# Kernel optimization log

Measured on AMD Instinct MI355X. Metric: run time of the kernel, lower is better.

The kernel has to match this reference:

```python
import jax, jax.numpy as jnp
import numpy as np

B, M, W, C, NN, J, ED, EMB = 8, 4096, 128, 32, 16, 4, 5, 2
EPS = 1e-5


def setup_inputs() -> dict:
    key = jax.random.key(0)
    ks = jax.random.split(key, 30)
    s = 0.05
    x = jax.random.normal(ks[0], (B, M, W), jnp.float32)
    pseudo = jax.random.normal(ks[1], (M * NN, EMB), jnp.float32)
    # structured indices: row r scatters its NN attention weights into row r of the m x m matrix
    nbr = jax.random.randint(ks[2], (M, NN), 0, M)
    L_idx = (jnp.arange(M)[:, None] * M + nbr).reshape(-1).astype(jnp.int32)
    inp = dict(x=x, pseudo=pseudo, L_idx=L_idx)
    inp['edge_w'] = jax.random.normal(ks[3], (ED, EMB), jnp.float32) * s
    inp['edge_b'] = jnp.zeros((ED,), jnp.float32)
    # Gaussian mixture params per layer (J components, encode_dim each); reset_parameters -> N(0,1)
    inp['mu0'] = jax.random.normal(ks[4], (J, ED), jnp.float32)
    inp['sigma0'] = jax.random.normal(ks[5], (J, ED), jnp.float32)
    inp['mu1'] = jax.random.normal(ks[6], (J, ED), jnp.float32)
    inp['sigma1'] = jax.random.normal(ks[7], (J, ED), jnp.float32)
    # layer 0: W -> C ; layer 1: C -> C
    inp['l1w0'] = jax.random.normal(ks[8], (C, W), jnp.float32) * s
    inp['l1b0'] = jnp.zeros((C,), jnp.float32)
    inp['l2w0'] = jax.random.normal(ks[9], (C, W), jnp.float32) * s
    inp['l2b0'] = jnp.zeros((C,), jnp.float32)
    inp['l1w1'] = jax.random.normal(ks[10], (C, C), jnp.float32) * s
    inp['l1b1'] = jnp.zeros((C,), jnp.float32)
    inp['l2w1'] = jax.random.normal(ks[11], (C, C), jnp.float32) * s
    inp['l2b1'] = jnp.zeros((C,), jnp.float32)
    inp['bn_g0'] = jnp.ones((C,), jnp.float32)
    inp['bn_b0'] = jnp.zeros((C,), jnp.float32)
    inp['bn_g1'] = jnp.ones((C,), jnp.float32)
    inp['bn_b1'] = jnp.zeros((C,), jnp.float32)
    inp['fc1w'] = jax.random.normal(ks[12], (256, M * C), jnp.float32) * 0.005
    inp['fc1b'] = jnp.zeros((256,), jnp.float32)
    inp['fc2w'] = jax.random.normal(ks[13], (53, 256), jnp.float32) * s
    inp['fc2b'] = jnp.zeros((53,), jnp.float32)
    return inp


def _get_L(pseudo, L_idx, edge_w, edge_b, mu, sigma, dtype):
    # Gaussian-mixture edge attention: u^T diag(sigma) u per component, summed, exp(-0.5 *)
    emb = pseudo @ edge_w.T + edge_b                      # (E, ED), E = M*NN
    u = emb[None, :, :] - mu[:, None, :]                  # (J, E, ED)
    q = jnp.sum(u * u * sigma[:, None, :], axis=-1)       # (J, E)
    w = jnp.sum(jnp.exp(-0.5 * q), axis=0)                # (E,)
    attn = jax.nn.softmax(w.reshape(M, NN), axis=1).reshape(-1)
    return jnp.zeros(M * M, dtype).at[L_idx].set(attn).reshape(M, M)


def _layer(x, L, w1, b1, w2, b2, g, bb):
    Lx = jnp.einsum('mn,bnf->bmf', L, x)                  # graph conv
    h = Lx @ w1.T + b1 + x @ w2.T + b2                    # (B, M, C)
    # BatchNorm1d (training mode): stats over batch and node dims, biased variance
    mean = jnp.mean(h, axis=(0, 1))
    var = jnp.var(h, axis=(0, 1))
    h = (h - mean) * jax.lax.rsqrt(var + EPS) * g + bb
    return jax.nn.relu(h)


def reference(x, pseudo, L_idx, edge_w, edge_b, mu0, sigma0, mu1, sigma1,
              l1w0, l1b0, l2w0, l2b0, l1w1, l1b1, l2w1, l2b1,
              bn_g0, bn_b0, bn_g1, bn_b1, fc1w, fc1b, fc2w, fc2b):
    L0 = _get_L(pseudo, L_idx, edge_w, edge_b, mu0, sigma0, x.dtype)
    h = _layer(x, L0, l1w0, l1b0, l2w0, l2b0, bn_g0, bn_b0)
    L1 = _get_L(pseudo, L_idx, edge_w, edge_b, mu1, sigma1, x.dtype)
    h = _layer(h, L1, l1w1, l1b1, l2w1, l2b1, bn_g1, bn_b1)
    flat = h.reshape(B, M * C)
    out = jax.nn.relu(flat @ fc1w.T + fc1b)               # dropout = identity (eval)
    return out @ fc2w.T + fc2b                            # (B, 53)
```

## Files before the change

### kernel.cpp

```cpp
#include <hip/hip_runtime.h>
#include <hip/hip_cooperative_groups.h>

namespace cg = cooperative_groups;

#define B_ 8
#define M_ 4096
#define W_ 128
#define C_ 32
#define NN_ 16

typedef short s16x8 __attribute__((ext_vector_type(8)));
typedef float f32x4 __attribute__((ext_vector_type(4)));

static __device__ __forceinline__ unsigned short f2bf(float f) {
  unsigned u = __builtin_bit_cast(unsigned, f);
  u = u + 0x7FFFu + ((u >> 16) & 1u);
  return (unsigned short)(u >> 16);
}
static __device__ __forceinline__ s16x8 cvt8v(float4 a, float4 b) {
  s16x8 r;
  r[0] = (short)f2bf(a.x); r[1] = (short)f2bf(a.y);
  r[2] = (short)f2bf(a.z); r[3] = (short)f2bf(a.w);
  r[4] = (short)f2bf(b.x); r[5] = (short)f2bf(b.y);
  r[6] = (short)f2bf(b.z); r[7] = (short)f2bf(b.w);
  return r;
}
static __device__ __forceinline__ float safeexp(float a) {
  return expf(fminf(a, 87.f));
}

__global__ void poison_kernel(float* __restrict__ out, int n, float val) {
  int t = blockIdx.x * blockDim.x + threadIdx.x;
  if (t < n) out[t] = val;
}


static __device__ void attn_row(
    int m, const float* __restrict__ pseudo, const int* __restrict__ Lidx,
    const float* __restrict__ edge_w, const float* __restrict__ edge_b,
    const float* __restrict__ mu0, const float* __restrict__ sg0,
    const float* __restrict__ mu1, const float* __restrict__ sg1,
    float* __restrict__ we0, float* __restrict__ we1, int* __restrict__ colb) {
  float w0[NN_], w1[NN_];
  int col[NN_];
#pragma unroll
  for (int n = 0; n < NN_; n++) {
    int e = m * NN_ + n;
    float p0 = pseudo[e * 2], p1 = pseudo[e * 2 + 1];
    float emb[5];
#pragma unroll
    for (int d = 0; d < 5; d++)
      emb[d] = p0 * edge_w[d * 2] + p1 * edge_w[d * 2 + 1] + edge_b[d];
    float a0 = 0.f, a1 = 0.f;
#pragma unroll
    for (int j = 0; j < 4; j++) {
      float qa = 0.f, qb = 0.f;
#pragma unroll
      for (int d = 0; d < 5; d++) {
        float u0 = emb[d] - mu0[j * 5 + d];
        qa += u0 * u0 * sg0[j * 5 + d];
        float u1 = emb[d] - mu1[j * 5 + d];
        qb += u1 * u1 * sg1[j * 5 + d];
      }
      a0 += safeexp(-0.5f * qa);
      a1 += safeexp(-0.5f * qb);
    }
    w0[n] = a0; w1[n] = a1;
    col[n] = Lidx[e] % M_;
  }
  float mx0 = w0[0], mx1 = w1[0];
#pragma unroll
  for (int n = 1; n < NN_; n++) { mx0 = fmaxf(mx0, w0[n]); mx1 = fmaxf(mx1, w1[n]); }
  float s0 = 0.f, s1 = 0.f;
#pragma unroll
  for (int n = 0; n < NN_; n++) {
    w0[n] = safeexp(w0[n] - mx0); s0 += w0[n];
    w1[n] = safeexp(w1[n] - mx1); s1 += w1[n];
  }
  float r0 = 1.f / s0, r1 = 1.f / s1;
#pragma unroll
  for (int n = 0; n < NN_; n++) {
    bool last = true;
#pragma unroll
    for (int n2 = n + 1; n2 < NN_; n2++)
      if (col[n2] == col[n]) last = false;
    int e = m * NN_ + n;
    we0[e] = last ? w0[n] * r0 : 0.f;
    we1[e] = last ? w1[n] * r1 : 0.f;
    colb[e] = col[n];
  }
}

static __device__ void proj0_tile(
    int blk, int tid, const float* __restrict__ x, const float* __restrict__ l1w0,
    const float* __restrict__ l2w0, float* __restrict__ G) {
  int lane = tid & 63, wave = tid >> 6;
  int l16 = lane & 15, quad = lane >> 4;
  int tile = blk * 4 + wave;
  f32x4 acc[4];
#pragma unroll
  for (int ct = 0; ct < 4; ct++) acc[ct] = (f32x4){0.f, 0.f, 0.f, 0.f};
  int row = tile * 16 + l16;
  const float* xr = x + (size_t)row * 128 + quad * 8;
  int out0 = l16;
#pragma unroll
  for (int kit = 0; kit < 4; kit++) {
    const float* ap = xr + kit * 32;
    s16x8 a = cvt8v(*(const float4*)ap, *(const float4*)(ap + 4));
#pragma unroll
    for (int ct = 0; ct < 4; ct++) {
      int out = ct * 16 + out0;
      const float* src = (out < 32 ? l1w0 + out * 128 : l2w0 + (out - 32) * 128)
                         + kit * 32 + quad * 8;
      s16x8 bf = cvt8v(*(const float4*)src, *(const float4*)(src + 4));
      acc[ct] = __builtin_amdgcn_mfma_f32_16x16x32_bf16(a, bf, acc[ct], 0, 0, 0);
    }
  }
  int rbase = tile * 16 + quad * 4;
#pragma unroll
  for (int ct = 0; ct < 4; ct++)
#pragma unroll
    for (int i = 0; i < 4; i++)
      G[(size_t)(rbase + i) * 64 + ct * 16 + l16] = acc[ct][i];
}

static __device__ void conv_block(
    int cb, int tid, char* smem,
    const float* __restrict__ G, const float* __restrict__ we,
    const int* __restrict__ colb, const float* __restrict__ b1c,
    const float* __restrict__ b2c, float* __restrict__ h,
    float* __restrict__ bns, float* __restrict__ bnq) {
  float (*s_we)[16] = (float(*)[16])smem;
  int   (*s_cn)[16] = (int(*)[16])(smem + 512);
  float* s_s = (float*)(smem + 1024);
  float* s_q = (float*)(smem + 1152);
  if (tid < 128) {
    int row = tid >> 4, nn = tid & 15;
    int m = (cb * 8 + row) & 4095;
    s_we[row][nn] = we[m * 16 + nn];
    s_cn[row][nn] = colb[m * 16 + nn];
  } else if (tid < 160) {
    s_s[tid - 128] = 0.f;
    s_q[tid - 128] = 0.f;
  }
  __syncthreads();
  int row = tid >> 5, c = tid & 31;
  int r = cb * 8 + row;
  int b = r >> 12;
  const float* Gb = G + ((size_t)b << 18);
  float acc = 0.f;
#pragma unroll
  for (int nn = 0; nn < NN_; nn++)
    acc += s_we[row][nn] * Gb[s_cn[row][nn] * 64 + c];
  float hv = acc + G[(size_t)r * 64 + 32 + c] + b1c[c] + b2c[c];
  h[(size_t)r * 32 + c] = hv;
  atomicAdd(&s_s[c], hv);
  atomicAdd(&s_q[c], hv * hv);
  __syncthreads();
  if (tid < 32) {
    int slot = cb & 255;
    atomicAdd(&bns[tid * 256 + slot], s_s[tid]);
    atomicAdd(&bnq[tid * 256 + slot], s_q[tid]);
  }
}

static __device__ void bnfin_block(
    int tid, char* smem, const float* __restrict__ bns, const float* __restrict__ bnq,
    const float* __restrict__ g, const float* __restrict__ bb,
    float* __restrict__ scale, float* __restrict__ shift) {
  float (*red)[8][32] = (float(*)[8][32])smem;
  int c = tid & 31, part = tid >> 5;
  float s = 0.f, q = 0.f;
#pragma unroll 8
  for (int i = 0; i < 32; i++) {
    s += bns[c * 256 + part * 32 + i];
    q += bnq[c * 256 + part * 32 + i];
  }
  red[0][part][c] = s;
  red[1][part][c] = q;
  __syncthreads();
  if (tid < 32) {
    float S = 0.f, Q = 0.f;
#pragma unroll
    for (int p = 0; p < 8; p++) { S += red[0][p][tid]; Q += red[1][p][tid]; }
    float mean = S * (1.f / 32768.f);
    float var = fmaxf(Q * (1.f / 32768.f) - mean * mean, 0.f);
    float sc = g[tid] * rsqrtf(var + 1e-5f);
    scale[tid] = sc;
    shift[tid] = bb[tid] - mean * sc;
  }
}

static __device__ void proj1_tile(
    int blk, int tid, const float* __restrict__ h0, const float* __restrict__ sc0,
    const float* __restrict__ l1w1, const float* __restrict__ l2w1,
    float* __restrict__ G) {
  int lane = tid & 63, wave = tid >> 6;
  int l16 = lane & 15, quad = lane >> 4;
  int tile = blk * 4 + wave;
  int row = tile * 16 + l16;
  const float* hr = h0 + (size_t)row * 32 + quad * 8;
  float4 hv0 = *(const float4*)hr;
  float4 hv1 = *(const float4*)(hr + 4);
  float av[8] = {hv0.x, hv0.y, hv0.z, hv0.w, hv1.x, hv1.y, hv1.z, hv1.w};
  s16x8 a;
#pragma unroll
  for (int j = 0; j < 8; j++) {
    float scv = sc0[quad * 8 + j];
    float shv = sc0[32 + quad * 8 + j];
    a[j] = (short)f2bf(fmaxf(av[j] * scv + shv, 0.f));
  }
  f32x4 acc[4];
#pragma unroll
  for (int ct = 0; ct < 4; ct++) {
    int out = ct * 16 + l16;
    const float* src = (out < 32 ? l1w1 + out * 32 : l2w1 + (out - 32) * 32) + quad * 8;
    s16x8 bf = cvt8v(*(const float4*)src, *(const float4*)(src + 4));
    f32x4 z = {0.f, 0.f, 0.f, 0.f};
    acc[ct] = __builtin_amdgcn_mfma_f32_16x16x32_bf16(a, bf, z, 0, 0, 0);
  }
  int rbase = tile * 16 + quad * 4;
#pragma unroll
  for (int ct = 0; ct < 4; ct++)
#pragma unroll
    for (int i = 0; i < 4; i++)
      G[(size_t)(rbase + i) * 64 + ct * 16 + l16] = acc[ct][i];
}

static __device__ void fc1_block(
    int u, int tid, char* smem, const float* __restrict__ h1,
    const float* __restrict__ sc1, const float* __restrict__ fc1w,
    float* __restrict__ fc1acc) {
  short* als = (short*)smem;
  int kc = u >> 2;
  int og = u & 3;
  size_t kbase = (size_t)kc << 9;
  for (int s = tid; s < 2048; s += 256) {
    int rowb = s >> 7;
    int k4 = (s & 127) << 2;
    short4 v4 = {0, 0, 0, 0};
    if (rowb < 8) {
      float4 hv = *(const float4*)(h1 + ((size_t)rowb << 17) + kbase + k4);
      int c = k4 & 31;
      float4 scv = *(const float4*)(sc1 + c);
      float4 shv = *(const float4*)(sc1 + 32 + c);
      v4.x = (short)f2bf(fmaxf(hv.x * scv.x + shv.x, 0.f));
      v4.y = (short)f2bf(fmaxf(hv.y * scv.y + shv.y, 0.f));
      v4.z = (short)f2bf(fmaxf(hv.z * scv.z + shv.z, 0.f));
      v4.w = (short)f2bf(fmaxf(hv.w * scv.w + shv.w, 0.f));
    }
    int byte = ((rowb << 10) + (k4 << 1)) ^ ((rowb & 7) << 4);
    *(short4*)((char*)als + byte) = v4;
  }
  __syncthreads();
  int lane = tid & 63, wave = tid >> 6;
  int l16 = lane & 15, quad = lane >> 4;
  int o = og * 64 + wave * 16 + l16;
  const float* wr = fc1w + (size_t)o * 131072 + kbase + quad * 8;
  int abase = (l16 << 10) + (quad << 4);
  int axor = (l16 & 7) << 4;
  f32x4 acc = {0.f, 0.f, 0.f, 0.f};
#pragma unroll 4
  for (int kk = 0; kk < 16; kk++) {
    const float* wp = wr + kk * 32;
    s16x8 bfr = cvt8v(*(const float4*)wp, *(const float4*)(wp + 4));
    s16x8 afr = *(const s16x8*)((const char*)als + ((abase + (kk << 6)) ^ axor));
    acc = __builtin_amdgcn_mfma_f32_16x16x32_bf16(afr, bfr, acc, 0, 0, 0);
  }
  if (quad < 2) {
#pragma unroll
    for (int i = 0; i < 4; i++)
      atomicAdd(&fc1acc[(quad * 4 + i) * 256 + o], acc[i]);
  }
  __syncthreads();
}

static __device__ void fc2_elem(
    int t, const float* __restrict__ fc1acc, const float* __restrict__ fc2w,
    const float* __restrict__ fc2b, float* __restrict__ out) {
  int b = t / 53, j = t - b * 53;
  float s = fc2b[j];
  const float* fa = fc1acc + b * 256;
  const float* wr = fc2w + j * 256;
#pragma unroll 8
  for (int o = 0; o < 256; o++) s += fmaxf(fa[o], 0.f) * wr[o];
  out[t] = s;
}

static __device__ __forceinline__ void prefetch_q(
    const float* __restrict__ fc1w, int quarter, int idx, int stride) {
  const float4* p = (const float4*)fc1w + (size_t)quarter * 2097152;
  float acc = 0.f;
  for (int i = idx; i < 2097152; i += stride) {
    float4 v = p[i];
    acc += v.x + v.y + v.z + v.w;
  }
  asm volatile("" :: "v"(acc));
}

__global__ __launch_bounds__(256, 4) void fused_kernel(
    const float* __restrict__ x, const float* __restrict__ pseudo,
    const int* __restrict__ Lidx,
    const float* __restrict__ edge_w, const float* __restrict__ edge_b,
    const float* __restrict__ mu0, const float* __restrict__ sg0,
    const float* __restrict__ mu1, const float* __restrict__ sg1,
    const float* __restrict__ l1w0, const float* __restrict__ l1b0,
    const float* __restrict__ l2w0, const float* __restrict__ l2b0,
    const float* __restrict__ l1w1, const float* __restrict__ l1b1,
    const float* __restrict__ l2w1, const float* __restrict__ l2b1,
    const float* __restrict__ bng0, const float* __restrict__ bnb0,
    const float* __restrict__ bng1, const float* __restrict__ bnb1,
    const float* __restrict__ fc1w, const float* __restrict__ fc1b,
    const float* __restrict__ fc2w, const float* __restrict__ fc2b,
    float* __restrict__ out,
    int* __restrict__ colb, float* __restrict__ we0, float* __restrict__ we1,
    float* __restrict__ G, float* __restrict__ h,
    float* __restrict__ bn, float* __restrict__ sc, float* __restrict__ fc1acc) {
  __shared__ char smem[16384];
  cg::grid_group grid = cg::this_grid();
  int bid = blockIdx.x, tid = threadIdx.x;
  int gtid = bid * 256 + tid;

  if (gtid < 2048) fc1acc[gtid] = fc1b[gtid & 255];
  else if (gtid < 34816) bn[gtid - 2048] = 0.f;
  if (bid < 16)
    attn_row(gtid, pseudo, Lidx, edge_w, edge_b, mu0, sg0, mu1, sg1, we0, we1, colb);
  grid.sync();

  if (bid < 512) proj0_tile(bid, tid, x, l1w0, l2w0, G);
  else           prefetch_q(fc1w, 0, (bid - 512) * 256 + tid, 131072);
  grid.sync();

  for (int it = 0; it < 4; it++) {
    __syncthreads();
    conv_block(bid + it * 1024, tid, smem, G, we0, colb, l1b0, l2b0,
               h, bn, bn + 8192);
  }
  prefetch_q(fc1w, 1, gtid, 262144);
  grid.sync();

  if (bid == 0) bnfin_block(tid, smem, bn, bn + 8192, bng0, bnb0, sc, sc + 32);
  else          prefetch_q(fc1w, 2, gtid - 256, 261888);
  grid.sync();

  if (bid < 512) proj1_tile(bid, tid, h, sc, l1w1, l2w1, G);
  else           prefetch_q(fc1w, 3, (bid - 512) * 256 + tid, 131072);
  grid.sync();

  for (int it = 0; it < 4; it++) {
    __syncthreads();
    conv_block(bid + it * 1024, tid, smem, G, we1, colb, l1b1, l2b1,
               h, bn + 16384, bn + 24576);
  }
  grid.sync();

  if (bid == 0) bnfin_block(tid, smem, bn + 16384, bn + 24576, bng1, bnb1,
                            sc + 64, sc + 96);
  grid.sync();

  fc1_block(bid, tid, smem, h, sc + 64, fc1w, fc1acc);
  grid.sync();

  if (gtid < 424) fc2_elem(gtid, fc1acc, fc2w, fc2b, out);
}

__global__ __launch_bounds__(256) void init_kernel(
    float* __restrict__ fc1acc, const float* __restrict__ fc1b,
    float* __restrict__ bn) {
  int g = blockIdx.x * 256 + threadIdx.x;
  if (g < 2048) fc1acc[g] = fc1b[g & 255];
  else if (g < 34816) bn[g - 2048] = 0.f;
}

__global__ __launch_bounds__(256) void attn_kernel(
    const float* __restrict__ pseudo, const int* __restrict__ Lidx,
    const float* __restrict__ edge_w, const float* __restrict__ edge_b,
    const float* __restrict__ mu0, const float* __restrict__ sg0,
    const float* __restrict__ mu1, const float* __restrict__ sg1,
    float* __restrict__ we0, float* __restrict__ we1, int* __restrict__ colb) {
  int m = blockIdx.x * 256 + threadIdx.x;
  if (m < M_)
    attn_row(m, pseudo, Lidx, edge_w, edge_b, mu0, sg0, mu1, sg1, we0, we1, colb);
}

__global__ __launch_bounds__(256) void proj0_kernel(
    const float* __restrict__ x, const float* __restrict__ l1w0,
    const float* __restrict__ l2w0, float* __restrict__ G) {
  proj0_tile(blockIdx.x, threadIdx.x, x, l1w0, l2w0, G);
}

__global__ __launch_bounds__(256) void conv_kernel(
    const float* __restrict__ G,
    const float* __restrict__ we, const int* __restrict__ colb,
    const float* __restrict__ b1c, const float* __restrict__ b2c,
    float* __restrict__ h, float* __restrict__ bns, float* __restrict__ bnq) {
  __shared__ char smem[1280];
  conv_block(blockIdx.x, threadIdx.x, smem, G, we, colb, b1c, b2c, h, bns, bnq);
}

__global__ __launch_bounds__(256) void bnfin_kernel(
    const float* __restrict__ bns, const float* __restrict__ bnq,
    const float* __restrict__ g, const float* __restrict__ bb,
    float* __restrict__ scale, float* __restrict__ shift) {
  __shared__ char smem[2048];
  bnfin_block(threadIdx.x, smem, bns, bnq, g, bb, scale, shift);
}

__global__ __launch_bounds__(256) void proj1_kernel(
    const float* __restrict__ h0, const float* __restrict__ sc0,
    const float* __restrict__ l1w1, const float* __restrict__ l2w1,
    float* __restrict__ G) {
  proj1_tile(blockIdx.x, threadIdx.x, h0, sc0, l1w1, l2w1, G);
}

__global__ __launch_bounds__(256) void fc1_kernel(
    const float* __restrict__ h1, const float* __restrict__ sc1,
    const float* __restrict__ fc1w, float* __restrict__ fc1acc) {
  __shared__ char smem[16384];
  fc1_block(blockIdx.x, threadIdx.x, smem, h1, sc1, fc1w, fc1acc);
}

__global__ void fc2_kernel(const float* __restrict__ fc1acc,
                           const float* __restrict__ fc2w,
                           const float* __restrict__ fc2b,
                           float* __restrict__ out) {
  int t = blockIdx.x * blockDim.x + threadIdx.x;
  if (t < 424) fc2_elem(t, fc1acc, fc2w, fc2b, out);
}

extern "C" void kernel_launch(void* const* d_in, const int* in_sizes, int n_in,
                              void* d_out, int out_size, void* d_ws, size_t ws_size,
                              hipStream_t stream) {
  float* out = (float*)d_out;
  int bad = 0;
  if (n_in != 25) bad = 2;
  else if (in_sizes[0] != 4194304) bad = 3;
  else if (in_sizes[2] != 65536) bad = 4;
  else if (in_sizes[21] != 33554432) bad = 5;
  else if (out_size != 424) bad = 6;
  else if (ws_size < 13509120) bad = 1;
  if (bad) {
    poison_kernel<<<2, 256, 0, stream>>>(out, out_size, (float)bad * 1.0e6f);
    return;
  }

  const float* x      = (const float*)d_in[0];
  const float* pseudo = (const float*)d_in[1];
  const int*   Lidx   = (const int*)d_in[2];
  const float* edge_w = (const float*)d_in[3];
  const float* edge_b = (const float*)d_in[4];
  const float* mu0    = (const float*)d_in[5];
  const float* sg0    = (const float*)d_in[6];
  const float* mu1    = (const float*)d_in[7];
  const float* sg1    = (const float*)d_in[8];
  const float* l1w0   = (const float*)d_in[9];
  const float* l1b0   = (const float*)d_in[10];
  const float* l2w0   = (const float*)d_in[11];
  const float* l2b0   = (const float*)d_in[12];
  const float* l1w1   = (const float*)d_in[13];
  const float* l1b1   = (const float*)d_in[14];
  const float* l2w1   = (const float*)d_in[15];
  const float* l2b1   = (const float*)d_in[16];
  const float* bng0   = (const float*)d_in[17];
  const float* bnb0   = (const float*)d_in[18];
  const float* bng1   = (const float*)d_in[19];
  const float* bnb1   = (const float*)d_in[20];
  const float* fc1w   = (const float*)d_in[21];
  const float* fc1b   = (const float*)d_in[22];
  const float* fc2w   = (const float*)d_in[23];
  const float* fc2b   = (const float*)d_in[24];

  char* Wp = (char*)d_ws;
  int*   colb   = (int*)  (Wp + 0);
  float* we0    = (float*)(Wp + 262144);
  float* we1    = (float*)(Wp + 524288);
  float* G      = (float*)(Wp + 786432);
  float* h0     = (float*)(Wp + 9175040);
  float* bn     = (float*)(Wp + 13369344);
  float* sc     = (float*)(Wp + 13500416);
  float* fc1acc = (float*)(Wp + 13500928);

  int maxb = 0;
  hipError_t oe = hipOccupancyMaxActiveBlocksPerMultiprocessor(&maxb, fused_kernel, 256, 0);
  bool coop = (oe == hipSuccess && maxb >= 4);
  if (coop) {
    void* args[] = {
      (void*)&x, (void*)&pseudo, (void*)&Lidx, (void*)&edge_w, (void*)&edge_b,
      (void*)&mu0, (void*)&sg0, (void*)&mu1, (void*)&sg1,
      (void*)&l1w0, (void*)&l1b0, (void*)&l2w0, (void*)&l2b0,
      (void*)&l1w1, (void*)&l1b1, (void*)&l2w1, (void*)&l2b1,
      (void*)&bng0, (void*)&bnb0, (void*)&bng1, (void*)&bnb1,
      (void*)&fc1w, (void*)&fc1b, (void*)&fc2w, (void*)&fc2b,
      (void*)&out,
      (void*)&colb, (void*)&we0, (void*)&we1, (void*)&G, (void*)&h0,
      (void*)&bn, (void*)&sc, (void*)&fc1acc };
    hipError_t le = hipLaunchCooperativeKernel((const void*)fused_kernel,
                                               dim3(1024), dim3(256), args, 0, stream);
    if (le != hipSuccess) coop = false;
  }
  if (!coop) {
    init_kernel<<<136, 256, 0, stream>>>(fc1acc, fc1b, bn);
    attn_kernel<<<16, 256, 0, stream>>>(pseudo, Lidx, edge_w, edge_b,
                                        mu0, sg0, mu1, sg1, we0, we1, colb);
    proj0_kernel<<<512, 256, 0, stream>>>(x, l1w0, l2w0, G);
    conv_kernel<<<4096, 256, 0, stream>>>(G, we0, colb, l1b0, l2b0,
                                          h0, bn, bn + 8192);
    bnfin_kernel<<<1, 256, 0, stream>>>(bn, bn + 8192, bng0, bnb0, sc, sc + 32);
    proj1_kernel<<<512, 256, 0, stream>>>(h0, sc, l1w1, l2w1, G);
    conv_kernel<<<4096, 256, 0, stream>>>(G, we1, colb, l1b1, l2b1,
                                          h0, bn + 16384, bn + 24576);
    bnfin_kernel<<<1, 256, 0, stream>>>(bn + 16384, bn + 24576, bng1, bnb1,
                                        sc + 64, sc + 96);
    fc1_kernel<<<1024, 256, 0, stream>>>(h0, sc + 64, fc1w, fc1acc);
    fc2_kernel<<<2, 256, 0, stream>>>(fc1acc, fc2w, fc2b, out);
  }
}
```

Before: 340.6 us.

## Replace cooperative grid sync with custom atomic barrier and fewer grid phases

Drops the cooperative launch and cg grid.sync in favour of a hand-rolled generation-counter barrier, with counters zeroed by a separate init kernel. The number of grid-wide phases is cut: attention runs beside the first projection, and BatchNorm finalisation is recomputed redundantly in each block's shared memory instead of in a separate single-block phase. The fc1 weight prefetch is reorganised into two large sweeps. The barrier relies on all 1024 blocks being co-resident without a cooperative-launch guarantee, and its spin loop has a timeout that could break correctness if it expires.

```diff
diff --git a/kernel.cpp b/kernel.cpp
--- a/kernel.cpp
+++ b/kernel.cpp
@@ -1,13 +1,11 @@
 #include <hip/hip_runtime.h>
-#include <hip/hip_cooperative_groups.h>
-
-namespace cg = cooperative_groups;
 
 #define B_ 8
 #define M_ 4096
 #define W_ 128
 #define C_ 32
 #define NN_ 16
+#define NBLK 1024
 
 typedef short s16x8 __attribute__((ext_vector_type(8)));
 typedef float f32x4 __attribute__((ext_vector_type(4)));
@@ -32,6 +30,31 @@
 __global__ void poison_kernel(float* __restrict__ out, int n, float val) {
   int t = blockIdx.x * blockDim.x + threadIdx.x;
   if (t < n) out[t] = val;
+}
+
+static __device__ __forceinline__ void gridbar(unsigned* __restrict__ bar, int tid) {
+  __syncthreads();
+  if (tid == 0) {
+    unsigned* cnt = bar;
+    unsigned* gen = bar + 64;
+    unsigned g = __hip_atomic_load(gen, __ATOMIC_RELAXED, __HIP_MEMORY_SCOPE_AGENT);
+    __threadfence();
+    unsigned old = __hip_atomic_fetch_add(cnt, 1u, __ATOMIC_ACQ_REL,
+                                          __HIP_MEMORY_SCOPE_AGENT);
+    if (old == NBLK - 1) {
+      __hip_atomic_store(cnt, 0u, __ATOMIC_RELAXED, __HIP_MEMORY_SCOPE_AGENT);
+      __hip_atomic_fetch_add(gen, 1u, __ATOMIC_RELEASE, __HIP_MEMORY_SCOPE_AGENT);
+    } else {
+      int t = 0;
+      while (__hip_atomic_load(gen, __ATOMIC_ACQUIRE,
+                               __HIP_MEMORY_SCOPE_AGENT) == g) {
+        __builtin_amdgcn_s_sleep(4);
+        if (++t > (1 << 18)) break;
+      }
+    }
+    __threadfence();
+  }
+  __syncthreads();
 }
 
 
@@ -102,14 +125,13 @@
   for (int ct = 0; ct < 4; ct++) acc[ct] = (f32x4){0.f, 0.f, 0.f, 0.f};
   int row = tile * 16 + l16;
   const float* xr = x + (size_t)row * 128 + quad * 8;
-  int out0 = l16;
 #pragma unroll
   for (int kit = 0; kit < 4; kit++) {
     const float* ap = xr + kit * 32;
     s16x8 a = cvt8v(*(const float4*)ap, *(const float4*)(ap + 4));
 #pragma unroll
     for (int ct = 0; ct < 4; ct++) {
-      int out = ct * 16 + out0;
+      int out = ct * 16 + l16;
       const float* src = (out < 32 ? l1w0 + out * 128 : l2w0 + (out - 32) * 128)
                          + kit * 32 + quad * 8;
       s16x8 bf = cvt8v(*(const float4*)src, *(const float4*)(src + 4));
@@ -164,10 +186,10 @@
   }
 }
 
-static __device__ void bnfin_block(
+static __device__ void bnfin_local(
     int tid, char* smem, const float* __restrict__ bns, const float* __restrict__ bnq,
     const float* __restrict__ g, const float* __restrict__ bb,
-    float* __restrict__ scale, float* __restrict__ shift) {
+    float* __restrict__ s_sc) {
   float (*red)[8][32] = (float(*)[8][32])smem;
   int c = tid & 31, part = tid >> 5;
   float s = 0.f, q = 0.f;
@@ -186,9 +208,10 @@
     float mean = S * (1.f / 32768.f);
     float var = fmaxf(Q * (1.f / 32768.f) - mean * mean, 0.f);
     float sc = g[tid] * rsqrtf(var + 1e-5f);
-    scale[tid] = sc;
-    shift[tid] = bb[tid] - mean * sc;
-  }
+    s_sc[tid] = sc;
+    s_sc[32 + tid] = bb[tid] - mean * sc;
+  }
+  __syncthreads();
 }
 
 static __device__ void proj1_tile(
@@ -272,7 +295,6 @@
     for (int i = 0; i < 4; i++)
       atomicAdd(&fc1acc[(quad * 4 + i) * 256 + o], acc[i]);
   }
-  __syncthreads();
 }
 
 static __device__ void fc2_elem(
@@ -287,15 +309,23 @@
   out[t] = s;
 }
 
-static __device__ __forceinline__ void prefetch_q(
-    const float* __restrict__ fc1w, int quarter, int idx, int stride) {
-  const float4* p = (const float4*)fc1w + (size_t)quarter * 2097152;
+static __device__ __forceinline__ void prefetch_range(
+    const float4* __restrict__ p, int n, int idx, int stride) {
   float acc = 0.f;
-  for (int i = idx; i < 2097152; i += stride) {
+  for (int i = idx; i < n; i += stride) {
     float4 v = p[i];
     acc += v.x + v.y + v.z + v.w;
   }
   asm volatile("" :: "v"(acc));
+}
+
+__global__ __launch_bounds__(256) void init_kernel(
+    float* __restrict__ fc1acc, const float* __restrict__ fc1b,
+    float* __restrict__ bn, unsigned* __restrict__ bar) {
+  int g = blockIdx.x * 256 + threadIdx.x;
+  if (g < 2048) fc1acc[g] = fc1b[g & 255];
+  else if (g < 34816) bn[g - 2048] = 0.f;
+  else if (g < 34944) bar[g - 34816] = 0u;
 }
 
 __global__ __launch_bounds__(256, 4) void fused_kernel(
@@ -310,122 +340,56 @@
     const float* __restrict__ l2w1, const float* __restrict__ l2b1,
     const float* __restrict__ bng0, const float* __restrict__ bnb0,
     const float* __restrict__ bng1, const float* __restrict__ bnb1,
-    const float* __restrict__ fc1w, const float* __restrict__ fc1b,
-    const float* __restrict__ fc2w, const float* __restrict__ fc2b,
+    const float* __restrict__ fc1w, const float* __restrict__ fc2w,
+    const float* __restrict__ fc2b,
     float* __restrict__ out,
     int* __restrict__ colb, float* __restrict__ we0, float* __restrict__ we1,
     float* __restrict__ G, float* __restrict__ h,
-    float* __restrict__ bn, float* __restrict__ sc, float* __restrict__ fc1acc) {
-  __shared__ char smem[16384];
-  cg::grid_group grid = cg::this_grid();
+    float* __restrict__ bn, float* __restrict__ fc1acc,
+    unsigned* __restrict__ bar) {
+  __shared__ char smem[16640];
+  float* s_sc = (float*)(smem + 16384);
   int bid = blockIdx.x, tid = threadIdx.x;
-  int gtid = bid * 256 + tid;
-
-  if (gtid < 2048) fc1acc[gtid] = fc1b[gtid & 255];
-  else if (gtid < 34816) bn[gtid - 2048] = 0.f;
-  if (bid < 16)
-    attn_row(gtid, pseudo, Lidx, edge_w, edge_b, mu0, sg0, mu1, sg1, we0, we1, colb);
-  grid.sync();
-
-  if (bid < 512) proj0_tile(bid, tid, x, l1w0, l2w0, G);
-  else           prefetch_q(fc1w, 0, (bid - 512) * 256 + tid, 131072);
-  grid.sync();
+
+  if (bid < 512) {
+    proj0_tile(bid, tid, x, l1w0, l2w0, G);
+  } else if (bid < 528) {
+    attn_row((bid - 512) * 256 + tid, pseudo, Lidx, edge_w, edge_b,
+             mu0, sg0, mu1, sg1, we0, we1, colb);
+  } else {
+    prefetch_range((const float4*)fc1w, 4194304, (bid - 528) * 256 + tid, 126976);
+  }
+  gridbar(bar, tid);
 
   for (int it = 0; it < 4; it++) {
     __syncthreads();
     conv_block(bid + it * 1024, tid, smem, G, we0, colb, l1b0, l2b0,
                h, bn, bn + 8192);
   }
-  prefetch_q(fc1w, 1, gtid, 262144);
-  grid.sync();
-
-  if (bid == 0) bnfin_block(tid, smem, bn, bn + 8192, bng0, bnb0, sc, sc + 32);
-  else          prefetch_q(fc1w, 2, gtid - 256, 261888);
-  grid.sync();
-
-  if (bid < 512) proj1_tile(bid, tid, h, sc, l1w1, l2w1, G);
-  else           prefetch_q(fc1w, 3, (bid - 512) * 256 + tid, 131072);
-  grid.sync();
+  gridbar(bar, tid);
+
+  if (bid < 512) {
+    bnfin_local(tid, smem, bn, bn + 8192, bng0, bnb0, s_sc);
+    proj1_tile(bid, tid, h, s_sc, l1w1, l2w1, G);
+  } else {
+    prefetch_range((const float4*)fc1w + 4194304, 4194304,
+                   (bid - 512) * 256 + tid, 131072);
+  }
+  gridbar(bar, tid);
 
   for (int it = 0; it < 4; it++) {
     __syncthreads();
     conv_block(bid + it * 1024, tid, smem, G, we1, colb, l1b1, l2b1,
                h, bn + 16384, bn + 24576);
   }
-  grid.sync();
-
-  if (bid == 0) bnfin_block(tid, smem, bn + 16384, bn + 24576, bng1, bnb1,
-                            sc + 64, sc + 96);
-  grid.sync();
-
-  fc1_block(bid, tid, smem, h, sc + 64, fc1w, fc1acc);
-  grid.sync();
-
+  gridbar(bar, tid);
+
+  bnfin_local(tid, smem, bn + 16384, bn + 24576, bng1, bnb1, s_sc);
+  fc1_block(bid, tid, smem, h, s_sc, fc1w, fc1acc);
+  gridbar(bar, tid);
+
+  int gtid = bid * 256 + tid;
   if (gtid < 424) fc2_elem(gtid, fc1acc, fc2w, fc2b, out);
-}
-
-__global__ __launch_bounds__(256) void init_kernel(
-    float* __restrict__ fc1acc, const float* __restrict__ fc1b,
-    float* __restrict__ bn) {
-  int g = blockIdx.x * 256 + threadIdx.x;
-  if (g < 2048) fc1acc[g] = fc1b[g & 255];
-  else if (g < 34816) bn[g - 2048] = 0.f;
-}
-
-__global__ __launch_bounds__(256) void attn_kernel(
-    const float* __restrict__ pseudo, const int* __restrict__ Lidx,
-    const float* __restrict__ edge_w, const float* __restrict__ edge_b,
-    const float* __restrict__ mu0, const float* __restrict__ sg0,
-    const float* __restrict__ mu1, const float* __restrict__ sg1,
-    float* __restrict__ we0, float* __restrict__ we1, int* __restrict__ colb) {
-  int m = blockIdx.x * 256 + threadIdx.x;
-  if (m < M_)
-    attn_row(m, pseudo, Lidx, edge_w, edge_b, mu0, sg0, mu1, sg1, we0, we1, colb);
-}
-
-__global__ __launch_bounds__(256) void proj0_kernel(
-    const float* __restrict__ x, const float* __restrict__ l1w0,
-    const float* __restrict__ l2w0, float* __restrict__ G) {
-  proj0_tile(blockIdx.x, threadIdx.x, x, l1w0, l2w0, G);
-}
-
-__global__ __launch_bounds__(256) void conv_kernel(
-    const float* __restrict__ G,
-    const float* __restrict__ we, const int* __restrict__ colb,
-    const float* __restrict__ b1c, const float* __restrict__ b2c,
-    float* __restrict__ h, float* __restrict__ bns, float* __restrict__ bnq) {
-  __shared__ char smem[1280];
-  conv_block(blockIdx.x, threadIdx.x, smem, G, we, colb, b1c, b2c, h, bns, bnq);
-}
-
-__global__ __launch_bounds__(256) void bnfin_kernel(
-    const float* __restrict__ bns, const float* __restrict__ bnq,
-    const float* __restrict__ g, const float* __restrict__ bb,
-    float* __restrict__ scale, float* __restrict__ shift) {
-  __shared__ char smem[2048];
-  bnfin_block(threadIdx.x, smem, bns, bnq, g, bb, scale, shift);
-}
-
-__global__ __launch_bounds__(256) void proj1_kernel(
-    const float* __restrict__ h0, const float* __restrict__ sc0,
-    const float* __restrict__ l1w1, const float* __restrict__ l2w1,
-    float* __restrict__ G) {
-  proj1_tile(blockIdx.x, threadIdx.x, h0, sc0, l1w1, l2w1, G);
-}
-
-__global__ __launch_bounds__(256) void fc1_kernel(
-    const float* __restrict__ h1, const float* __restrict__ sc1,
-    const float* __restrict__ fc1w, float* __restrict__ fc1acc) {
-  __shared__ char smem[16384];
-  fc1_block(blockIdx.x, threadIdx.x, smem, h1, sc1, fc1w, fc1acc);
-}
-
-__global__ void fc2_kernel(const float* __restrict__ fc1acc,
-                           const float* __restrict__ fc2w,
-                           const float* __restrict__ fc2b,
-                           float* __restrict__ out) {
-  int t = blockIdx.x * blockDim.x + threadIdx.x;
-  if (t < 424) fc2_elem(t, fc1acc, fc2w, fc2b, out);
 }
 
 extern "C" void kernel_launch(void* const* d_in, const int* in_sizes, int n_in,
@@ -438,7 +402,7 @@
   else if (in_sizes[2] != 65536) bad = 4;
   else if (in_sizes[21] != 33554432) bad = 5;
   else if (out_size != 424) bad = 6;
-  else if (ws_size < 13509120) bad = 1;
+  else if (ws_size < 13509632) bad = 1;
   if (bad) {
     poison_kernel<<<2, 256, 0, stream>>>(out, out_size, (float)bad * 1.0e6f);
     return;
@@ -471,47 +435,19 @@
   const float* fc2b   = (const float*)d_in[24];
 
   char* Wp = (char*)d_ws;
-  int*   colb   = (int*)  (Wp + 0);
-  float* we0    = (float*)(Wp + 262144);
-  float* we1    = (float*)(Wp + 524288);
-  float* G      = (float*)(Wp + 786432);
-  float* h0     = (float*)(Wp + 9175040);
-  float* bn     = (float*)(Wp + 13369344);
-  float* sc     = (float*)(Wp + 13500416);
-  float* fc1acc = (float*)(Wp + 13500928);
-
-  int maxb = 0;
-  hipError_t oe = hipOccupancyMaxActiveBlocksPerMultiprocessor(&maxb, fused_kernel, 256, 0);
-  bool coop = (oe == hipSuccess && maxb >= 4);
-  if (coop) {
-    void* args[] = {
-      (void*)&x, (void*)&pseudo, (void*)&Lidx, (void*)&edge_w, (void*)&edge_b,
-      (void*)&mu0, (void*)&sg0, (void*)&mu1, (void*)&sg1,
-      (void*)&l1w0, (void*)&l1b0, (void*)&l2w0, (void*)&l2b0,
-      (void*)&l1w1, (void*)&l1b1, (void*)&l2w1, (void*)&l2b1,
-      (void*)&bng0, (void*)&bnb0, (void*)&bng1, (void*)&bnb1,
-      (void*)&fc1w, (void*)&fc1b, (void*)&fc2w, (void*)&fc2b,
-      (void*)&out,
-      (void*)&colb, (void*)&we0, (void*)&we1, (void*)&G, (void*)&h0,
-      (void*)&bn, (void*)&sc, (void*)&fc1acc };
-    hipError_t le = hipLaunchCooperativeKernel((const void*)fused_kernel,
-                                               dim3(1024), dim3(256), args, 0, stream);
-    if (le != hipSuccess) coop = false;
-  }
-  if (!coop) {
-    init_kernel<<<136, 256, 0, stream>>>(fc1acc, fc1b, bn);
-    attn_kernel<<<16, 256, 0, stream>>>(pseudo, Lidx, edge_w, edge_b,
-                                        mu0, sg0, mu1, sg1, we0, we1, colb);
-    proj0_kernel<<<512, 256, 0, stream>>>(x, l1w0, l2w0, G);
-    conv_kernel<<<4096, 256, 0, stream>>>(G, we0, colb, l1b0, l2b0,
-                                          h0, bn, bn + 8192);
-    bnfin_kernel<<<1, 256, 0, stream>>>(bn, bn + 8192, bng0, bnb0, sc, sc + 32);
-    proj1_kernel<<<512, 256, 0, stream>>>(h0, sc, l1w1, l2w1, G);
-    conv_kernel<<<4096, 256, 0, stream>>>(G, we1, colb, l1b1, l2b1,
-                                          h0, bn + 16384, bn + 24576);
-    bnfin_kernel<<<1, 256, 0, stream>>>(bn + 16384, bn + 24576, bng1, bnb1,
-                                        sc + 64, sc + 96);
-    fc1_kernel<<<1024, 256, 0, stream>>>(h0, sc + 64, fc1w, fc1acc);
-    fc2_kernel<<<2, 256, 0, stream>>>(fc1acc, fc2w, fc2b, out);
-  }
-}
+  int*      colb   = (int*)     (Wp + 0);
+  float*    we0    = (float*)   (Wp + 262144);
+  float*    we1    = (float*)   (Wp + 524288);
+  float*    G      = (float*)   (Wp + 786432);
+  float*    h0     = (float*)   (Wp + 9175040);
+  float*    bn     = (float*)   (Wp + 13369344);
+  float*    fc1acc = (float*)   (Wp + 13500928);
+  unsigned* bar    = (unsigned*)(Wp + 13509120);
+
+  init_kernel<<<137, 256, 0, stream>>>(fc1acc, fc1b, bn, bar);
+  fused_kernel<<<1024, 256, 0, stream>>>(
+      x, pseudo, Lidx, edge_w, edge_b, mu0, sg0, mu1, sg1,
+      l1w0, l1b0, l2w0, l2b0, l1w1, l1b1, l2w1, l2b1,
+      bng0, bnb0, bng1, bnb1, fc1w, fc2w, fc2b, out,
+      colb, we0, we1, G, h0, bn, fc1acc, bar);
+}
```

Result: slower. 1.344 ms (+294.7%).
